# Performance work log

Measured on AMD Instinct MI355X. Metric: run time of the kernel, lower is better.

## Reference

```python
import jax, jax.numpy as jnp
import numpy as np

H, B, S, D, T = 4, 16, 2048, 128, 5  # n_head, batch, seq_len, d_model, num event types
BAND_K = 64  # latest-k band width, as in get_latest_k_mask


def setup_inputs() -> dict:
    key = jax.random.key(0)
    ks = jax.random.split(key, 5)
    output = jax.random.normal(ks[0], (B, S, D), dtype=jnp.float32)
    # banded 'latest-k' mask: mask[i, i:i+k] = 1  (start=max(i,i-k+1)=i, end=min(S,i+k))
    i = jnp.arange(S)
    band = ((i[None, :] >= i[:, None]) & (i[None, :] < i[:, None] + BAND_K)).astype(jnp.float32)
    local_cor = band[None]  # [1, S, S]
    cor_matrix = jax.random.normal(ks[1], (T, D), dtype=jnp.float32)
    event_type = jax.random.randint(ks[2], (B, S), 1, T + 1)  # 1-based event ids in [1, T]
    # per-head linear3 params (xavier-ish); self.linear is unused in forward
    W3 = jax.random.normal(ks[3], (H, D, D), dtype=jnp.float32) / np.sqrt(D)
    b3 = jnp.zeros((H, D), dtype=jnp.float32)
    return dict(output=output, local_cor=local_cor, cor_matrix=cor_matrix,
                event_type=event_type, W3=W3, b3=b3)


def reference(output, local_cor, cor_matrix, event_type, W3, b3):
    # (corr^T @ cor_matrix[et-1]).mean(2) == einsum('bsd,bs->bd', corr, cor_matrix[et-1].mean(-1))
    g = cor_matrix.mean(-1)[event_type - 1]  # [B, S]
    x = output
    sum_seq = jnp.zeros_like(output)          # sum over heads of [B,S,D]
    sum_head = jnp.zeros((output.shape[0], output.shape[2]), output.dtype)  # [B,D]
    for h in range(H):
        z = jax.nn.elu(jnp.einsum('bsd,ed->bse', x, W3[h]) + b3[h])  # linear3 + ELU
        corr = jnp.matmul(local_cor, z)       # [1,S,S] @ [B,S,D] -> [B,S,D]
        head_out = jnp.einsum('bsd,bs->bd', corr, g)  # [B,D]
        sum_seq = sum_seq + corr
        sum_head = sum_head + head_out
        x = corr                               # next head consumes correlation_output
    return (sum_seq, sum_head)
```

## Files before the change

### kernel.cpp

```cpp
#include <hip/hip_runtime.h>
#include <math.h>

#define NHEAD 4
#define BATCH 16
#define SEQ   2048
#define DMODEL 128
#define NTYPES 5
#define BAND  64
#define MROWS (BATCH * SEQ)

typedef __attribute__((ext_vector_type(8))) short bf16x8;
typedef __attribute__((ext_vector_type(4))) float f32x4;
typedef __attribute__((ext_vector_type(4))) unsigned int u32x4;

static __device__ __forceinline__ unsigned short f2bf(float f) {
  unsigned int u = __float_as_uint(f);
  unsigned int r = (u + 0x7fffu + ((u >> 16) & 1u)) >> 16;
  return (unsigned short)r;
}
static __device__ __forceinline__ float bflo(unsigned int v) {
  return __uint_as_float(v << 16);
}
static __device__ __forceinline__ float bfhi(unsigned int v) {
  return __uint_as_float(v & 0xffff0000u);
}
static __device__ __forceinline__ unsigned int pkbf(float lo, float hi) {
  return ((unsigned int)f2bf(hi) << 16) | (unsigned int)f2bf(lo);
}
static __device__ __forceinline__ float elu(float v) {
  const float ev = __expf(fminf(v, 0.f)) - 1.f;
  return v > 0.f ? v : ev;
}
static __device__ __forceinline__ int xcd_swz(int blk, int nwg) {
  return (blk & 7) * (nwg >> 3) + (blk >> 3);
}

__global__ __launch_bounds__(512, 4) void gemm0_kernel(
    const float* __restrict__ X0,
    const float* __restrict__ W3,
    const float* __restrict__ bvec,
    unsigned short* __restrict__ Zb,
    float* __restrict__ SH,
    unsigned short* __restrict__ wbf) {
  __shared__ __align__(16) char lds[64 * 272 + 128 * 272];
  char* Xl = lds;
  char* Wl = lds + 64 * 272;
  const int tid = threadIdx.x;
  const int swz = xcd_swz(blockIdx.x, gridDim.x);
  const int row0 = swz * 64;

  if (blockIdx.x < 16 && tid < DMODEL) SH[blockIdx.x * DMODEL + tid] = 0.f;
  if (blockIdx.x < 12) {
    const long u = (long)(blockIdx.x * 512 + tid) * 8 + DMODEL * DMODEL;
    float4 a = *reinterpret_cast<const float4*>(W3 + u);
    float4 c = *reinterpret_cast<const float4*>(W3 + u + 4);
    unsigned short o[8];
    o[0] = f2bf(a.x); o[1] = f2bf(a.y); o[2] = f2bf(a.z); o[3] = f2bf(a.w);
    o[4] = f2bf(c.x); o[5] = f2bf(c.y); o[6] = f2bf(c.z); o[7] = f2bf(c.w);
    *reinterpret_cast<u32x4*>(wbf + u) = *reinterpret_cast<u32x4*>(o);
  }

  #pragma unroll
  for (int it = 0; it < 2; ++it) {
    const int u = it * 512 + tid;
    const int r = u >> 4, g4 = u & 15;
    const float* xs = X0 + (long)(row0 + r) * DMODEL + g4 * 8;
    float4 f0 = *reinterpret_cast<const float4*>(xs);
    float4 f1 = *reinterpret_cast<const float4*>(xs + 4);
    unsigned short o[8];
    o[0] = f2bf(f0.x); o[1] = f2bf(f0.y); o[2] = f2bf(f0.z); o[3] = f2bf(f0.w);
    o[4] = f2bf(f1.x); o[5] = f2bf(f1.y); o[6] = f2bf(f1.z); o[7] = f2bf(f1.w);
    *reinterpret_cast<u32x4*>(Xl + r * 272 + g4 * 16) = *reinterpret_cast<u32x4*>(o);
  }
  #pragma unroll
  for (int it = 0; it < 4; ++it) {
    const int u = it * 512 + tid;
    const int e = u >> 4, g4 = u & 15;
    const float* wsrc = W3 + e * DMODEL + g4 * 8;
    float4 f0 = *reinterpret_cast<const float4*>(wsrc);
    float4 f1 = *reinterpret_cast<const float4*>(wsrc + 4);
    unsigned short o[8];
    o[0] = f2bf(f0.x); o[1] = f2bf(f0.y); o[2] = f2bf(f0.z); o[3] = f2bf(f0.w);
    o[4] = f2bf(f1.x); o[5] = f2bf(f1.y); o[6] = f2bf(f1.z); o[7] = f2bf(f1.w);
    *reinterpret_cast<u32x4*>(Wl + e * 272 + g4 * 16) = *reinterpret_cast<u32x4*>(o);
  }
  __syncthreads();

  const int wv = tid >> 6, l = tid & 63;
  const int mv = wv >> 1, nh = wv & 1;
  const int lr = l & 15, lk = l >> 4;
  f32x4 acc[4];
  #pragma unroll
  for (int n = 0; n < 4; ++n) acc[n] = (f32x4){0.f, 0.f, 0.f, 0.f};
  #pragma unroll
  for (int t = 0; t < 4; ++t) {
    const bf16x8 a = *reinterpret_cast<const bf16x8*>(
        Xl + (mv * 16 + lr) * 272 + (t * 4 + lk) * 16);
    #pragma unroll
    for (int n = 0; n < 4; ++n) {
      const bf16x8 bfrag = *reinterpret_cast<const bf16x8*>(
          Wl + (nh * 64 + n * 16 + lr) * 272 + (t * 4 + lk) * 16);
      acc[n] = __builtin_amdgcn_mfma_f32_16x16x32_bf16(a, bfrag, acc[n], 0, 0, 0);
    }
  }
  #pragma unroll
  for (int n = 0; n < 4; ++n) {
    const int col = nh * 64 + n * 16 + lr;
    const float bias = bvec[col];
    #pragma unroll
    for (int r = 0; r < 4; ++r) {
      const int row = row0 + mv * 16 + lk * 4 + r;
      Zb[(long)row * DMODEL + col] = f2bf(elu(acc[n][r] + bias));
    }
  }
}

template <int ACC>
__global__ __launch_bounds__(512, 4) void fused_band_gemm(
    const unsigned short* __restrict__ Zin,
    const unsigned short* __restrict__ CSin,
    unsigned short* __restrict__ Cout,
    const unsigned short* __restrict__ Wb,
    const float* __restrict__ bvec,
    unsigned short* __restrict__ Zout,
    float* __restrict__ SH,
    const int* __restrict__ et,
    const float* __restrict__ corm) {
  __shared__ __align__(16) char lds[64512];
  char* Xl = lds;
  char* Wl = lds + 17408;
  float2* s8 = reinterpret_cast<float2*>(lds + 52224);
  float* hred = reinterpret_cast<float*>(lds + 60416);
  float* rowmean = reinterpret_cast<float*>(Xl + 256);

  const int tid = threadIdx.x;
  const int swz = xcd_swz(blockIdx.x, gridDim.x);
  const int r0 = swz * 64;
  const int b = r0 >> 11, s0 = r0 & 2047;
  const int p = tid & 63, q = tid >> 6;

  const unsigned int* zsrc =
      reinterpret_cast<const unsigned int*>(Zin) + (long)b * SEQ * 64 + p;
  unsigned int zlo[8], zhi[8];
  int etr[8];
  #pragma unroll
  for (int i = 0; i < 8; ++i) {
    const int sl = s0 + q * 8 + i;
    zlo[i] = zsrc[(long)sl * 64];
    const int sh_ = sl + BAND;
    zhi[i] = (sh_ < SEQ) ? zsrc[(long)sh_ * 64] : 0u;
    etr[i] = et[(long)b * SEQ + sl];
  }
  unsigned int csr[8];
  if (ACC) {
    #pragma unroll
    for (int i = 0; i < 8; ++i)
      csr[i] = *reinterpret_cast<const unsigned int*>(
          CSin + ((long)r0 + q * 8 + i) * DMODEL + 2 * p);
  }
  #pragma unroll
  for (int it = 0; it < 4; ++it) {
    const int u = it * 512 + tid;
    const int e = u >> 4, g4 = u & 15;
    u32x4 v = *reinterpret_cast<const u32x4*>(Wb + e * DMODEL + g4 * 8);
    *reinterpret_cast<u32x4*>(Wl + e * 272 + g4 * 16) = v;
  }
  if (tid < 64) {
    #pragma unroll
    for (int t = 0; t < NTYPES; ++t) {
      float v = corm[t * DMODEL + tid] + corm[t * DMODEL + 64 + tid];
      #pragma unroll
      for (int o = 32; o > 0; o >>= 1) v += __shfl_xor(v, o, 64);
      if (tid == 0) rowmean[t * 68] = v * (1.0f / DMODEL);
    }
  }
  {
    float a0 = 0.f, a1 = 0.f, b0 = 0.f, b1 = 0.f;
    #pragma unroll
    for (int i = 0; i < 8; ++i) {
      a0 += bflo(zlo[i]); a1 += bfhi(zlo[i]);
      b0 += bflo(zhi[i]); b1 += bfhi(zhi[i]);
    }
    s8[q * 64 + p] = make_float2(a0, a1);
    s8[(q + 8) * 64 + p] = make_float2(b0, b1);
  }
  __syncthreads();

  float w0 = 0.f, w1 = 0.f;
  #pragma unroll
  for (int j = 0; j < 8; ++j) {
    const float2 v = s8[(q + j) * 64 + p];
    w0 += v.x; w1 += v.y;
  }
  float hs0 = 0.f, hs1 = 0.f;
  unsigned int pks[8];
  #pragma unroll
  for (int i = 0; i < 8; ++i) {
    const int s = q * 8 + i;
    const float c0v = w0, c1v = w1;
    const float g = rowmean[(etr[i] - 1) * 68];
    hs0 += c0v * g; hs1 += c1v * g;
    const unsigned int raw = pkbf(c0v, c1v);
    if (ACC)
      pks[i] = pkbf(c0v + bflo(csr[i]), c1v + bfhi(csr[i]));
    else
      pks[i] = raw;
    *reinterpret_cast<unsigned int*>(Xl + s * 272 + p * 4) = raw;
    w0 += bflo(zhi[i]) - bflo(zlo[i]);
    w1 += bfhi(zhi[i]) - bfhi(zlo[i]);
  }
  *reinterpret_cast<float2*>(hred + (p * 8 + q) * 2) = make_float2(hs0, hs1);
  __syncthreads();

  #pragma unroll
  for (int i = 0; i < 8; ++i)
    *reinterpret_cast<unsigned int*>(
        Cout + ((long)r0 + q * 8 + i) * DMODEL + 2 * p) = pks[i];
  if (q == 0) {
    float t0 = 0.f, t1 = 0.f;
    #pragma unroll
    for (int k = 0; k < 8; ++k) {
      const float2 v = *reinterpret_cast<const float2*>(hred + (p * 8 + k) * 2);
      t0 += v.x; t1 += v.y;
    }
    atomicAdd(SH + b * DMODEL + 2 * p, t0);
    atomicAdd(SH + b * DMODEL + 2 * p + 1, t1);
  }
  const int wv = tid >> 6, l = tid & 63;
  const int mv = wv >> 1, nh = wv & 1;
  const int lr = l & 15, lk = l >> 4;
  f32x4 acc[4];
  #pragma unroll
  for (int n = 0; n < 4; ++n) acc[n] = (f32x4){0.f, 0.f, 0.f, 0.f};
  #pragma unroll
  for (int t = 0; t < 4; ++t) {
    const bf16x8 a = *reinterpret_cast<const bf16x8*>(
        Xl + (mv * 16 + lr) * 272 + (t * 4 + lk) * 16);
    #pragma unroll
    for (int n = 0; n < 4; ++n) {
      const bf16x8 bfrag = *reinterpret_cast<const bf16x8*>(
          Wl + (nh * 64 + n * 16 + lr) * 272 + (t * 4 + lk) * 16);
      acc[n] = __builtin_amdgcn_mfma_f32_16x16x32_bf16(a, bfrag, acc[n], 0, 0, 0);
    }
  }
  #pragma unroll
  for (int n = 0; n < 4; ++n) {
    const int col = nh * 64 + n * 16 + lr;
    const float bias = bvec[col];
    #pragma unroll
    for (int r = 0; r < 4; ++r) {
      const int row = r0 + mv * 16 + lk * 4 + r;
      Zout[(long)row * DMODEL + col] = f2bf(elu(acc[n][r] + bias));
    }
  }
}

__global__ __launch_bounds__(512, 4) void band3_kernel(
    const unsigned short* __restrict__ Zin,
    const unsigned short* __restrict__ CSin,
    float* __restrict__ SS,
    float* __restrict__ SH,
    const int* __restrict__ et,
    const float* __restrict__ corm) {
  __shared__ float2 s8[16 * 64];
  __shared__ float hred[64 * 8 * 2];
  __shared__ float rowmean[NTYPES];

  const int tid = threadIdx.x;
  const int swz = xcd_swz(blockIdx.x, gridDim.x);
  const int r0 = swz * 64;
  const int b = r0 >> 11, s0 = r0 & 2047;
  const int p = tid & 63, q = tid >> 6;

  const unsigned int* zsrc =
      reinterpret_cast<const unsigned int*>(Zin) + (long)b * SEQ * 64 + p;
  unsigned int zlo[8], zhi[8], csr[8];
  int etr[8];
  #pragma unroll
  for (int i = 0; i < 8; ++i) {
    const int sl = s0 + q * 8 + i;
    zlo[i] = zsrc[(long)sl * 64];
    const int sh_ = sl + BAND;
    zhi[i] = (sh_ < SEQ) ? zsrc[(long)sh_ * 64] : 0u;
    etr[i] = et[(long)b * SEQ + sl];
    csr[i] = *reinterpret_cast<const unsigned int*>(
        CSin + ((long)r0 + q * 8 + i) * DMODEL + 2 * p);
  }
  if (tid < 64) {
    #pragma unroll
    for (int t = 0; t < NTYPES; ++t) {
      float v = corm[t * DMODEL + tid] + corm[t * DMODEL + 64 + tid];
      #pragma unroll
      for (int o = 32; o > 0; o >>= 1) v += __shfl_xor(v, o, 64);
      if (tid == 0) rowmean[t] = v * (1.0f / DMODEL);
    }
  }
  {
    float a0 = 0.f, a1 = 0.f, b0 = 0.f, b1 = 0.f;
    #pragma unroll
    for (int i = 0; i < 8; ++i) {
      a0 += bflo(zlo[i]); a1 += bfhi(zlo[i]);
      b0 += bflo(zhi[i]); b1 += bfhi(zhi[i]);
    }
    s8[q * 64 + p] = make_float2(a0, a1);
    s8[(q + 8) * 64 + p] = make_float2(b0, b1);
  }
  __syncthreads();

  float w0 = 0.f, w1 = 0.f;
  #pragma unroll
  for (int j = 0; j < 8; ++j) {
    const float2 v = s8[(q + j) * 64 + p];
    w0 += v.x; w1 += v.y;
  }
  float hs0 = 0.f, hs1 = 0.f;
  unsigned long long ssv[8];
  #pragma unroll
  for (int i = 0; i < 8; ++i) {
    const float c0v = w0, c1v = w1;
    const float g = rowmean[etr[i] - 1];
    hs0 += c0v * g; hs1 += c1v * g;
    const float ox = c0v + bflo(csr[i]);
    const float oy = c1v + bfhi(csr[i]);
    ssv[i] = (unsigned long long)__float_as_uint(ox) |
             ((unsigned long long)__float_as_uint(oy) << 32);
    w0 += bflo(zhi[i]) - bflo(zlo[i]);
    w1 += bfhi(zhi[i]) - bfhi(zlo[i]);
  }
  *reinterpret_cast<float2*>(hred + (p * 8 + q) * 2) = make_float2(hs0, hs1);
  __syncthreads();

  if (q == 0) {
    float t0 = 0.f, t1 = 0.f;
    #pragma unroll
    for (int k = 0; k < 8; ++k) {
      const float2 v = *reinterpret_cast<const float2*>(hred + (p * 8 + k) * 2);
      t0 += v.x; t1 += v.y;
    }
    atomicAdd(SH + b * DMODEL + 2 * p, t0);
    atomicAdd(SH + b * DMODEL + 2 * p + 1, t1);
  }
  #pragma unroll
  for (int i = 0; i < 8; ++i)
    __builtin_nontemporal_store(
        ssv[i], reinterpret_cast<unsigned long long*>(
                    SS + ((long)r0 + q * 8 + i) * DMODEL + 2 * p));
}

extern "C" void kernel_launch(void* const* d_in, const int* in_sizes, int n_in,
                              void* d_out, int out_size, void* d_ws, size_t ws_size,
                              hipStream_t stream) {
  const float* x0   = (const float*)d_in[0];
  const float* corm = (const float*)d_in[2];
  const int*   et   = (const int*)d_in[3];
  const float* W3   = (const float*)d_in[4];
  const float* b3   = (const float*)d_in[5];

  float* out_ss = (float*)d_out;
  float* out_sh = out_ss + (size_t)MROWS * DMODEL;

  char* ws = (char*)d_ws;
  const size_t MB = 1024 * 1024;
  unsigned short* A = (unsigned short*)(ws + 0 * MB);
  unsigned short* B = (unsigned short*)(ws + 8 * MB);
  unsigned short* C = (unsigned short*)(ws + 16 * MB);
  unsigned short* D = (unsigned short*)(ws + 24 * MB);
  unsigned short* E = (unsigned short*)(ws + 32 * MB);
  unsigned short* wbf = (unsigned short*)(ws + 40 * MB);

  const size_t WSTR = (size_t)DMODEL * DMODEL;

  gemm0_kernel<<<512, 512, 0, stream>>>(x0, W3, b3, A, out_sh, wbf);
  fused_band_gemm<0><<<512, 512, 0, stream>>>(
      A, nullptr, B, wbf + 1 * WSTR, b3 + 1 * DMODEL, E, out_sh, et, corm);
  fused_band_gemm<1><<<512, 512, 0, stream>>>(
      E, B, C, wbf + 2 * WSTR, b3 + 2 * DMODEL, A, out_sh, et, corm);
  fused_band_gemm<1><<<512, 512, 0, stream>>>(
      A, C, D, wbf + 3 * WSTR, b3 + 3 * DMODEL, E, out_sh, et, corm);
  band3_kernel<<<512, 512, 0, stream>>>(E, D, out_ss, out_sh, et, corm);
}
```

Baseline: 53.90 us.

## Fuse last band-GEMM stage with final band kernel using halo recompute

Merges the third fused_band_gemm launch and band3_kernel into one kernel. Each block recomputes the 64-row halo of the head-3 GEMM input in LDS, so the head-3 z values never go through global memory. This drops one launch and one intermediate global write and read. In exchange the block does twice the MFMA work for its tile, needs about 70 KB of LDS (which lowers occupancy), and adds extra barriers.

```diff
diff --git a/kernel.cpp b/kernel.cpp
--- a/kernel.cpp
+++ b/kernel.cpp
@@ -255,16 +255,23 @@
   }
 }
 
-__global__ __launch_bounds__(512, 4) void band3_kernel(
+__global__ __launch_bounds__(512, 4) void f2final_kernel(
     const unsigned short* __restrict__ Zin,
     const unsigned short* __restrict__ CSin,
+    const unsigned short* __restrict__ Wb,
+    const float* __restrict__ bvec,
     float* __restrict__ SS,
     float* __restrict__ SH,
     const int* __restrict__ et,
     const float* __restrict__ corm) {
-  __shared__ float2 s8[16 * 64];
-  __shared__ float hred[64 * 8 * 2];
+  __shared__ __align__(16) char lds[71680];
   __shared__ float rowmean[NTYPES];
+  char* Xl = lds;
+  char* Wl = lds + 34816;
+  char* z3 = Wl;
+  float2* s8 = reinterpret_cast<float2*>(lds);
+  float2* s8v2 = reinterpret_cast<float2*>(lds);
+  float* hred = reinterpret_cast<float*>(lds + 69632);
 
   const int tid = threadIdx.x;
   const int swz = xcd_swz(blockIdx.x, gridDim.x);
@@ -274,17 +281,30 @@
 
   const unsigned int* zsrc =
       reinterpret_cast<const unsigned int*>(Zin) + (long)b * SEQ * 64 + p;
-  unsigned int zlo[8], zhi[8], csr[8];
-  int etr[8];
-  #pragma unroll
-  for (int i = 0; i < 8; ++i) {
-    const int sl = s0 + q * 8 + i;
-    zlo[i] = zsrc[(long)sl * 64];
+  unsigned int zlo[16], zhi[16];
+  #pragma unroll
+  for (int i = 0; i < 16; ++i) {
+    const int sl = s0 + q * 16 + i;
+    zlo[i] = (sl < SEQ) ? zsrc[(long)sl * 64] : 0u;
     const int sh_ = sl + BAND;
     zhi[i] = (sh_ < SEQ) ? zsrc[(long)sh_ * 64] : 0u;
-    etr[i] = et[(long)b * SEQ + sl];
-    csr[i] = *reinterpret_cast<const unsigned int*>(
-        CSin + ((long)r0 + q * 8 + i) * DMODEL + 2 * p);
+  }
+  unsigned int cs2p[16];
+  int etr[16];
+  if (q < 4) {
+    #pragma unroll
+    for (int i = 0; i < 16; ++i) {
+      cs2p[i] = *reinterpret_cast<const unsigned int*>(
+          CSin + ((long)r0 + q * 16 + i) * DMODEL + 2 * p);
+      etr[i] = et[(long)b * SEQ + s0 + q * 16 + i];
+    }
+  }
+  #pragma unroll
+  for (int it = 0; it < 4; ++it) {
+    const int u = it * 512 + tid;
+    const int e = u >> 4, g4 = u & 15;
+    u32x4 v = *reinterpret_cast<const u32x4*>(Wb + e * DMODEL + g4 * 8);
+    *reinterpret_cast<u32x4*>(Wl + e * 272 + g4 * 16) = v;
   }
   if (tid < 64) {
     #pragma unroll
@@ -300,51 +320,146 @@
     #pragma unroll
     for (int i = 0; i < 8; ++i) {
       a0 += bflo(zlo[i]); a1 += bfhi(zlo[i]);
-      b0 += bflo(zhi[i]); b1 += bfhi(zhi[i]);
-    }
-    s8[q * 64 + p] = make_float2(a0, a1);
-    s8[(q + 8) * 64 + p] = make_float2(b0, b1);
+      b0 += bflo(zlo[8 + i]); b1 += bfhi(zlo[8 + i]);
+    }
+    s8[(2 * q) * 64 + p] = make_float2(a0, a1);
+    s8[(2 * q + 1) * 64 + p] = make_float2(b0, b1);
+    if (q >= 4) {
+      float c0 = 0.f, c1 = 0.f, d0 = 0.f, d1 = 0.f;
+      #pragma unroll
+      for (int i = 0; i < 8; ++i) {
+        c0 += bflo(zhi[i]); c1 += bfhi(zhi[i]);
+        d0 += bflo(zhi[8 + i]); d1 += bfhi(zhi[8 + i]);
+      }
+      s8[(2 * q + 8) * 64 + p] = make_float2(c0, c1);
+      s8[(2 * q + 9) * 64 + p] = make_float2(d0, d1);
+    }
   }
   __syncthreads();
 
   float w0 = 0.f, w1 = 0.f;
   #pragma unroll
   for (int j = 0; j < 8; ++j) {
-    const float2 v = s8[(q + j) * 64 + p];
+    const float2 v = s8[(2 * q + j) * 64 + p];
     w0 += v.x; w1 += v.y;
   }
+  __syncthreads();
+
   float hs0 = 0.f, hs1 = 0.f;
-  unsigned long long ssv[8];
-  #pragma unroll
-  for (int i = 0; i < 8; ++i) {
+  #pragma unroll
+  for (int i = 0; i < 16; ++i) {
+    const int s = q * 16 + i;
     const float c0v = w0, c1v = w1;
-    const float g = rowmean[etr[i] - 1];
-    hs0 += c0v * g; hs1 += c1v * g;
-    const float ox = c0v + bflo(csr[i]);
-    const float oy = c1v + bfhi(csr[i]);
-    ssv[i] = (unsigned long long)__float_as_uint(ox) |
-             ((unsigned long long)__float_as_uint(oy) << 32);
+    if (q < 4) {
+      const float g = rowmean[etr[i] - 1];
+      hs0 += c0v * g; hs1 += c1v * g;
+      cs2p[i] = pkbf(c0v + bflo(cs2p[i]), c1v + bfhi(cs2p[i]));
+    }
+    *reinterpret_cast<unsigned int*>(Xl + s * 272 + p * 4) = pkbf(c0v, c1v);
     w0 += bflo(zhi[i]) - bflo(zlo[i]);
     w1 += bfhi(zhi[i]) - bfhi(zlo[i]);
   }
-  *reinterpret_cast<float2*>(hred + (p * 8 + q) * 2) = make_float2(hs0, hs1);
-  __syncthreads();
-
+  __syncthreads();
+
+  const int mv = q >> 1, nh = q & 1;
+  const int lr = tid & 15, lk = (tid & 63) >> 4;
+  f32x4 acc[2][4];
+  #pragma unroll
+  for (int h2 = 0; h2 < 2; ++h2)
+    #pragma unroll
+    for (int n = 0; n < 4; ++n) acc[h2][n] = (f32x4){0.f, 0.f, 0.f, 0.f};
+  #pragma unroll
+  for (int h2 = 0; h2 < 2; ++h2) {
+    #pragma unroll
+    for (int t = 0; t < 4; ++t) {
+      const bf16x8 a = *reinterpret_cast<const bf16x8*>(
+          Xl + (h2 * 64 + mv * 16 + lr) * 272 + (t * 4 + lk) * 16);
+      #pragma unroll
+      for (int n = 0; n < 4; ++n) {
+        const bf16x8 bfrag = *reinterpret_cast<const bf16x8*>(
+            Wl + (nh * 64 + n * 16 + lr) * 272 + (t * 4 + lk) * 16);
+        acc[h2][n] = __builtin_amdgcn_mfma_f32_16x16x32_bf16(a, bfrag,
+                                                             acc[h2][n], 0, 0, 0);
+      }
+    }
+  }
+  __syncthreads();
+
+  #pragma unroll
+  for (int h2 = 0; h2 < 2; ++h2) {
+    #pragma unroll
+    for (int n = 0; n < 4; ++n) {
+      const int col = nh * 64 + n * 16 + lr;
+      const float bias = bvec[col];
+      #pragma unroll
+      for (int r = 0; r < 4; ++r) {
+        const int row = h2 * 64 + mv * 16 + lk * 4 + r;
+        const float v = elu(acc[h2][n][r] + bias);
+        const unsigned short bz =
+            (s0 + row < SEQ) ? f2bf(v) : (unsigned short)0;
+        *reinterpret_cast<unsigned short*>(z3 + row * 260 + col * 2) = bz;
+      }
+    }
+  }
+  __syncthreads();
+
+  {
+    float a0 = 0.f, a1 = 0.f, b0 = 0.f, b1 = 0.f;
+    #pragma unroll
+    for (int jr = 0; jr < 8; ++jr) {
+      const unsigned int v0 = *reinterpret_cast<const unsigned int*>(
+          z3 + (2 * q * 8 + jr) * 260 + p * 4);
+      const unsigned int v1 = *reinterpret_cast<const unsigned int*>(
+          z3 + ((2 * q + 1) * 8 + jr) * 260 + p * 4);
+      a0 += bflo(v0); a1 += bfhi(v0);
+      b0 += bflo(v1); b1 += bfhi(v1);
+    }
+    s8v2[(2 * q) * 64 + p] = make_float2(a0, a1);
+    s8v2[(2 * q + 1) * 64 + p] = make_float2(b0, b1);
+  }
+  __syncthreads();
+
+  if (q < 4) {
+    float v0 = 0.f, v1 = 0.f;
+    #pragma unroll
+    for (int j = 0; j < 8; ++j) {
+      const float2 v = s8v2[(2 * q + j) * 64 + p];
+      v0 += v.x; v1 += v.y;
+    }
+    #pragma unroll
+    for (int i = 0; i < 16; ++i) {
+      const int s = q * 16 + i;
+      const float c3l = v0, c3h = v1;
+      const float g = rowmean[etr[i] - 1];
+      hs0 += c3l * g; hs1 += c3h * g;
+      const float ox = c3l + bflo(cs2p[i]);
+      const float oy = c3h + bfhi(cs2p[i]);
+      const unsigned long long sv =
+          (unsigned long long)__float_as_uint(ox) |
+          ((unsigned long long)__float_as_uint(oy) << 32);
+      __builtin_nontemporal_store(
+          sv, reinterpret_cast<unsigned long long*>(
+                  SS + ((long)r0 + s) * DMODEL + 2 * p));
+      const unsigned int va = *reinterpret_cast<const unsigned int*>(
+          z3 + (s + BAND) * 260 + p * 4);
+      const unsigned int vs = *reinterpret_cast<const unsigned int*>(
+          z3 + s * 260 + p * 4);
+      v0 += bflo(va) - bflo(vs);
+      v1 += bfhi(va) - bfhi(vs);
+    }
+    *reinterpret_cast<float2*>(hred + (p * 4 + q) * 2) = make_float2(hs0, hs1);
+  }
+  __syncthreads();
   if (q == 0) {
     float t0 = 0.f, t1 = 0.f;
     #pragma unroll
-    for (int k = 0; k < 8; ++k) {
-      const float2 v = *reinterpret_cast<const float2*>(hred + (p * 8 + k) * 2);
+    for (int k = 0; k < 4; ++k) {
+      const float2 v = *reinterpret_cast<const float2*>(hred + (p * 4 + k) * 2);
       t0 += v.x; t1 += v.y;
     }
     atomicAdd(SH + b * DMODEL + 2 * p, t0);
     atomicAdd(SH + b * DMODEL + 2 * p + 1, t1);
   }
-  #pragma unroll
-  for (int i = 0; i < 8; ++i)
-    __builtin_nontemporal_store(
-        ssv[i], reinterpret_cast<unsigned long long*>(
-                    SS + ((long)r0 + q * 8 + i) * DMODEL + 2 * p));
 }
 
 extern "C" void kernel_launch(void* const* d_in, const int* in_sizes, int n_in,
@@ -364,9 +479,8 @@
   unsigned short* A = (unsigned short*)(ws + 0 * MB);
   unsigned short* B = (unsigned short*)(ws + 8 * MB);
   unsigned short* C = (unsigned short*)(ws + 16 * MB);
-  unsigned short* D = (unsigned short*)(ws + 24 * MB);
-  unsigned short* E = (unsigned short*)(ws + 32 * MB);
-  unsigned short* wbf = (unsigned short*)(ws + 40 * MB);
+  unsigned short* E = (unsigned short*)(ws + 24 * MB);
+  unsigned short* wbf = (unsigned short*)(ws + 32 * MB);
 
   const size_t WSTR = (size_t)DMODEL * DMODEL;
 
@@ -375,7 +489,6 @@
       A, nullptr, B, wbf + 1 * WSTR, b3 + 1 * DMODEL, E, out_sh, et, corm);
   fused_band_gemm<1><<<512, 512, 0, stream>>>(
       E, B, C, wbf + 2 * WSTR, b3 + 2 * DMODEL, A, out_sh, et, corm);
-  fused_band_gemm<1><<<512, 512, 0, stream>>>(
-      A, C, D, wbf + 3 * WSTR, b3 + 3 * DMODEL, E, out_sh, et, corm);
-  band3_kernel<<<512, 512, 0, stream>>>(E, D, out_ss, out_sh, et, corm);
-}
+  f2final_kernel<<<512, 512, 0, stream>>>(
+      A, C, wbf + 3 * WSTR, b3 + 3 * DMODEL, out_ss, out_sh, et, corm);
+}
```

Result: faster. 51.92 us (median of 2 runs) (-3.7%).
